# Kernel tuning notes

Hardware: AMD Instinct MI355X
Metric: run time of the kernel (lower is better)

## Reference

```python
import jax, jax.numpy as jnp
import numpy as np

D = 128; H = 4; DK = D // H; ZN = 64; V = 8

def _silu(x):
    return x * jax.nn.sigmoid(x)

def _mlp3(x, w1, b1, w2, b2, w3, b3):
    h = _silu(x @ w1 + b1)
    h = _silu(h @ w2 + b2)
    return h @ w3 + b3

def _snorm(x):
    # StaticLayerNorm: center, divide by unbiased std (torch .std default ddof=1)
    c = x - jnp.mean(x, axis=-1, keepdims=True)
    std = jnp.sqrt(jnp.sum(c * c, axis=-1, keepdims=True) / (x.shape[-1] - 1))
    std = jnp.where(std == 0, 1.0, std)
    return c / std

def setup_inputs():
    key = jax.random.key(0)
    ks = list(jax.random.split(key, 40)); ki = iter(ks)
    xs = (6.0 / (DK + D)) ** 0.5
    inp = {}
    inp["latent"] = jax.random.normal(next(ki), (ZN, D, V, V, V), jnp.float32)
    inp["nodes"] = jax.random.normal(next(ki), (ZN, D), jnp.float32)
    inp["t"] = jax.random.uniform(next(ki), (ZN,), jnp.float32)
    for nm in ("qw", "kw", "vw"):
        inp[nm] = jax.random.uniform(next(ki), (H, D, DK), jnp.float32, -xs, xs)
    for nm in ("qb", "kb", "vb"):
        inp[nm] = jnp.zeros((H, DK), jnp.float32)
    inp["ow"] = jax.random.normal(next(ki), (D, D), jnp.float32) * (1.0 / D) ** 0.5
    for pre, dout in (("an_gb", 2 * D), ("an_a", D), ("fn_gb", 2 * D), ("fn_a", D)):
        inp[pre + "_w1"] = jax.random.normal(next(ki), (D, D), jnp.float32) * 0.05
        inp[pre + "_b1"] = jnp.zeros((D,), jnp.float32)
        inp[pre + "_w2"] = jax.random.normal(next(ki), (D, D), jnp.float32) * 0.05
        inp[pre + "_b2"] = jnp.zeros((D,), jnp.float32)
        inp[pre + "_w3"] = jax.random.normal(next(ki), (D, dout), jnp.float32) * 0.05
        inp[pre + "_b3"] = jnp.zeros((dout,), jnp.float32)
    return inp

def reference(latent, nodes, t, qw, kw, vw, qb, kb, vb, ow,
              an_gb_w1, an_gb_b1, an_gb_w2, an_gb_b2, an_gb_w3, an_gb_b3,
              an_a_w1, an_a_b1, an_a_w2, an_a_b2, an_a_w3, an_a_b3,
              fn_gb_w1, fn_gb_b1, fn_gb_w2, fn_gb_b2, fn_gb_w3, fn_gb_b3,
              fn_a_w1, fn_a_b1, fn_a_w2, fn_a_b2, fn_a_w3, fn_a_b3):
    b, d, vx, vy, vz = latent.shape
    n = vx * vy * vz
    x = latent.reshape(b, d, n).transpose(0, 2, 1)  # [b, n, d]
    cond = nodes[:, None, :] + t[:, None, None]     # [b, 1, d]
    gb1 = _mlp3(cond, an_gb_w1, an_gb_b1, an_gb_w2, an_gb_b2, an_gb_w3, an_gb_b3)
    g1, be1 = jnp.split(gb1, 2, axis=-1)
    al1 = _mlp3(cond, an_a_w1, an_a_b1, an_a_w2, an_a_b2, an_a_w3, an_a_b3)
    gb2 = _mlp3(cond, fn_gb_w1, fn_gb_b1, fn_gb_w2, fn_gb_b2, fn_gb_w3, fn_gb_b3)
    g2, be2 = jnp.split(gb2, 2, axis=-1)
    al2 = _mlp3(cond, fn_a_w1, fn_a_b1, fn_a_w2, fn_a_b2, fn_a_w3, fn_a_b3)
    # FAITHFUL BUG REPRO: source unpacks adaLN's (gamma, beta, alpha) as (alpha, gamma, beta)
    alpha1, gamma1, beta1 = g1, be1, al1
    alpha2, gamma2, beta2 = g2, be2, al2
    x2 = gamma1 * _snorm(x) + beta1
    dk = d // qw.shape[0]
    Q = jnp.einsum('bnd,hdk->bhnk', x2, qw) + qb[None, :, None, :]
    K = jnp.einsum('bnd,hdk->bhnk', x2, kw) + kb[None, :, None, :]
    Vv = jnp.einsum('bnd,hdk->bhnk', x2, vw) + vb[None, :, None, :]
    S = jnp.einsum('bhnk,bhmk->bhnm', Q, K) / (dk ** 0.5)
    P = jax.nn.softmax(S, axis=-1)
    O = jnp.einsum('bhnm,bhmk->bhnk', P, Vv)
    O = O.transpose(0, 2, 3, 1).reshape(b, n, d)  # matches torch permute(0,2,3,1).reshape
    attn = O @ ow
    x = x + alpha1 * attn
    x2 = gamma2 * _snorm(x) + beta2
    x = x + alpha2 * x2  # NOTE: source forward never applies self.ffn (dead module)
    return x.transpose(0, 2, 1).reshape(b, d, vx, vy, vz)
```

## Files before the change

### kernel.cpp

```cpp
#include <hip/hip_runtime.h>
#include <hip/hip_bf16.h>
#include <math.h>


#define NB 64

typedef __attribute__((ext_vector_type(8))) short bf16x8;
typedef __attribute__((ext_vector_type(4))) float f32x4;

__device__ __forceinline__ float silu_f(float x) { return x / (1.0f + __expf(-x)); }
__device__ __forceinline__ unsigned short f2bf(float x) {
    __hip_bfloat16 h = __float2bfloat16(x);
    return *reinterpret_cast<unsigned short*>(&h);
}

__global__ void __launch_bounds__(128) k_cond(
    const float* __restrict__ nodes, const float* __restrict__ tv,
    const float* __restrict__ w10, const float* __restrict__ b10,
    const float* __restrict__ w20, const float* __restrict__ b20,
    const float* __restrict__ w30, const float* __restrict__ b30,
    const float* __restrict__ w11, const float* __restrict__ b11,
    const float* __restrict__ w21, const float* __restrict__ b21,
    const float* __restrict__ w31, const float* __restrict__ b31,
    const float* __restrict__ w12, const float* __restrict__ b12,
    const float* __restrict__ w22, const float* __restrict__ b22,
    const float* __restrict__ w32, const float* __restrict__ b32,
    const float* __restrict__ w13, const float* __restrict__ b13,
    const float* __restrict__ w23, const float* __restrict__ b23,
    const float* __restrict__ w33, const float* __restrict__ b33,
    float* __restrict__ mods,
    const float* __restrict__ qw, const float* __restrict__ kw,
    const float* __restrict__ vw, const float* __restrict__ ow,
    unsigned short* __restrict__ cT, unsigned short* __restrict__ owT)
{
    int blk = blockIdx.x;
    int t = threadIdx.x;

    if (blk >= NB*4) {
        int pbase = (blk - NB*4)*128 + t;
        #pragma unroll
        for (int rep = 0; rep < 2; rep++) {
            int idx = pbase + rep*32768;
            if (idx < 49152) {
                int ph = idx >> 14, r = idx & 16383, c = r >> 7, d = r & 127;
                int h = c >> 5, kk = c & 31;
                const float* wp = ph==0 ? qw : (ph==1 ? kw : vw);
                cT[idx] = f2bf(wp[h*4096 + d*32 + kk]);
            } else {
                int r = idx - 49152, c = r >> 7, i = r & 127;
                owT[r] = f2bf(ow[i*128 + c]);
            }
        }
        return;
    }

    int b = blk >> 2, m = blk & 3;
    const float* W1 = m==0?w10 : m==1?w11 : m==2?w12 : w13;
    const float* B1 = m==0?b10 : m==1?b11 : m==2?b12 : b13;
    const float* W2 = m==0?w20 : m==1?w21 : m==2?w22 : w23;
    const float* B2 = m==0?b20 : m==1?b21 : m==2?b22 : b23;
    const float* W3 = m==0?w30 : m==1?w31 : m==2?w32 : w33;
    const float* B3 = m==0?b30 : m==1?b31 : m==2?b32 : b33;
    int dout256 = (m == 0 || m == 2);
    int slot = (m==0)?0 : (m==1)?2 : (m==2)?3 : 5;

    __shared__ float xs[128], h1[128], h2[128];
    xs[t] = nodes[b*128 + t] + tv[b];
    __syncthreads();

    float acc = B1[t];
    for (int i = 0; i < 128; i++) acc += xs[i] * W1[i*128 + t];
    h1[t] = silu_f(acc);
    __syncthreads();

    acc = B2[t];
    for (int i = 0; i < 128; i++) acc += h1[i] * W2[i*128 + t];
    h2[t] = silu_f(acc);
    __syncthreads();

    if (dout256) {
        float a0 = B3[t], a1 = B3[t + 128];
        for (int i = 0; i < 128; i++) {
            float h = h2[i];
            a0 += h * W3[i*256 + t];
            a1 += h * W3[i*256 + t + 128];
        }
        mods[((size_t)b*6 + slot    )*128 + t] = a0;
        mods[((size_t)b*6 + slot + 1)*128 + t] = a1;
    } else {
        float a0 = B3[t];
        for (int i = 0; i < 128; i++) a0 += h2[i] * W3[i*128 + t];
        mods[((size_t)b*6 + slot)*128 + t] = a0;
    }
}

__global__ void __launch_bounds__(256, 3) k_norm_qkv(
    const float* __restrict__ latent, const float* __restrict__ mods,
    const unsigned short* __restrict__ cT,
    const float* __restrict__ qb, const float* __restrict__ kb, const float* __restrict__ vb,
    unsigned short* __restrict__ Qb, unsigned short* __restrict__ Kb,
    unsigned short* __restrict__ Vtb)
{
    __shared__ unsigned short xb[64*136];
    __shared__ unsigned short WtS[128*136];

    int blk = blockIdx.x;
    int b = blk >> 3, n0 = (blk & 7) * 64;
    int t = threadIdx.x;
    int j = t >> 2, sub = t & 3;

    const float* lp = latent + (size_t)b*65536 + n0 + j;
    float lat[32];
    #pragma unroll
    for (int i = 0; i < 32; i++)
        lat[i] = lp[(size_t)(sub*32 + i)*512];

    float s = 0.f, ss = 0.f;
    #pragma unroll
    for (int i = 0; i < 32; i++) { s += lat[i]; ss += lat[i]*lat[i]; }
    s += __shfl_xor(s, 1); ss += __shfl_xor(ss, 1);
    s += __shfl_xor(s, 2); ss += __shfl_xor(ss, 2);
    float mean = s * (1.0f/128.0f);
    float var = (ss - 128.0f*mean*mean) * (1.0f/127.0f);
    var = var < 0.f ? 0.f : var;
    float sd = sqrtf(var);
    float rstd = (sd == 0.f) ? 1.f : 1.f/sd;

    const float* g1p  = mods + ((size_t)b*6 + 1)*128 + sub*32;
    const float* be1p = mods + ((size_t)b*6 + 2)*128 + sub*32;
    unsigned int* xbw = (unsigned int*)xb + j*68 + sub*16;
    #pragma unroll
    for (int i2 = 0; i2 < 16; i2++) {
        float v0 = g1p[2*i2]   * ((lat[2*i2]   - mean)*rstd) + be1p[2*i2];
        float v1 = g1p[2*i2+1] * ((lat[2*i2+1] - mean)*rstd) + be1p[2*i2+1];
        xbw[i2] = (unsigned)f2bf(v0) | ((unsigned)f2bf(v1) << 16);
    }
    __syncthreads();

    int w = t >> 6, lane = t & 63, lo = lane & 15, hi = lane >> 4;
    bf16x8 af[4];
    #pragma unroll
    for (int kc = 0; kc < 4; kc++)
        af[kc] = *(const bf16x8*)(xb + (w*16 + lo)*136 + kc*32 + hi*8);

    const f32x4 zero = {0.f, 0.f, 0.f, 0.f};
    const float qscale = 0.17677669529663687f * 1.4426950408889634f;
    unsigned int* WtSw = (unsigned int*)WtS;

    #pragma unroll 1
    for (int ph = 0; ph < 3; ph++) {
        __syncthreads();
        {
            const uint4* cq = (const uint4*)(cT + ph*16384);
            #pragma unroll
            for (int k = 0; k < 8; k++) {
                int idx4 = t + k*256;
                int c = idx4 >> 4, d2b = (idx4 & 15)*4;
                uint4 v = cq[idx4];
                *(uint4*)(WtSw + c*68 + d2b) = v;
            }
        }
        __syncthreads();

        for (int nt = 0; nt < 8; nt++) {
            f32x4 acc = zero;
            #pragma unroll
            for (int kc = 0; kc < 4; kc++) {
                bf16x8 bf = *(const bf16x8*)(WtS + (nt*16 + lo)*136 + kc*32 + hi*8);
                acc = __builtin_amdgcn_mfma_f32_16x16x32_bf16(af[kc], bf, acc, 0, 0, 0);
            }
            int c = nt*16 + lo, h = c >> 5, kk = c & 31;
            size_t bh = (size_t)(b*4 + h);
            if (ph == 0) {
                float bias = qb[c];
                #pragma unroll
                for (int jj = 0; jj < 4; jj++) {
                    int n = n0 + w*16 + hi*4 + jj;
                    Qb[(bh*512 + n)*32 + kk] = f2bf((acc[jj] + bias) * qscale);
                }
            } else if (ph == 1) {
                float bias = kb[c];
                #pragma unroll
                for (int jj = 0; jj < 4; jj++) {
                    int n = n0 + w*16 + hi*4 + jj;
                    Kb[(bh*512 + n)*32 + kk] = f2bf(acc[jj] + bias);
                }
            } else {
                float bias = vb[c];
                #pragma unroll
                for (int jj = 0; jj < 4; jj++) {
                    int nl = w*16 + hi*4 + jj;
                    xb[c*68 + nl] = f2bf(acc[jj] + bias);
                }
            }
        }
    }
    __syncthreads();
    for (int idx = t; idx < 8192; idx += 256) {
        int c = idx >> 6, jj = idx & 63;
        int h = c >> 5, kk = c & 31;
        size_t bh = (size_t)(b*4 + h);
        Vtb[(bh*32 + kk)*512 + n0 + jj] = xb[c*68 + jj];
    }
}

__global__ void __launch_bounds__(512, 4) k_attn(
    const unsigned short* __restrict__ Qb, const unsigned short* __restrict__ Kb,
    const unsigned short* __restrict__ Vtb, unsigned short* __restrict__ Ob)
{
    __shared__ unsigned short KsS[512*32];
    __shared__ unsigned short VsS[32*512];

    int blk = blockIdx.x;
    int bh = blk >> 1, qhalf = blk & 1;
    int t = threadIdx.x;

    const unsigned short* kgp = Kb + (size_t)bh*512*32;
    const unsigned short* vgp = Vtb + (size_t)bh*32*512;
    for (int idx = t; idx < 2048; idx += 512)
        *(bf16x8*)(KsS + idx*8) = *(const bf16x8*)(kgp + idx*8);
    for (int idx = t; idx < 2048; idx += 512) {
        int r = idx >> 6, cch = idx & 63;
        *(bf16x8*)(VsS + r*512 + ((cch*8) ^ ((r&7)<<3))) =
            *(const bf16x8*)(vgp + r*512 + cch*8);
    }
    __syncthreads();

    int w = t >> 6, lane = t & 63, lo = lane & 15, hi = lane >> 4;
    const unsigned short* qbase = Qb + (size_t)bh*512*32;
    const f32x4 zero = {0.f, 0.f, 0.f, 0.f};
    int b = bh >> 2, h = bh & 3;

    const unsigned short* Vl0 = VsS + lo*512;
    const unsigned short* Vl1 = VsS + (16 + lo)*512;
    int swz = (lo & 7) << 3;
    int srcA = lo + 32*(hi & 1);

    for (int qt = 0; qt < 2; ++qt) {
        int q0 = qhalf*256 + w*32 + qt*16;
        bf16x8 qa = *(const bf16x8*)(qbase + (size_t)(q0 + lo)*32 + hi*8);

        float m = -1e30f, sum = 0.f;
        f32x4 oa = zero, ob = zero;

        #pragma unroll 1
        for (int ch = 0; ch < 4; ++ch) {
            f32x4 s8[8];
            #pragma unroll
            for (int kt = 0; kt < 8; ++kt) {
                bf16x8 kf = *(const bf16x8*)(KsS + ((ch*8 + kt)*16 + lo)*32 + hi*8);
                s8[kt] = __builtin_amdgcn_mfma_f32_16x16x32_bf16(kf, qa, zero, 0, 0, 0);
            }

            float cm = -1e30f;
            #pragma unroll
            for (int kt = 0; kt < 8; ++kt)
                cm = fmaxf(cm, fmaxf(fmaxf(s8[kt][0], s8[kt][1]), fmaxf(s8[kt][2], s8[kt][3])));
            cm = fmaxf(cm, __shfl_xor(cm, 16));
            cm = fmaxf(cm, __shfl_xor(cm, 32));
            float nm = fmaxf(m, cm);
            float sc = __builtin_amdgcn_exp2f(m - nm);
            sum *= sc;
            #pragma unroll
            for (int jj = 0; jj < 4; ++jj) { oa[jj] *= sc; ob[jj] *= sc; }
            m = nm;

            unsigned pw0c[8], pw1c[8];
            #pragma unroll
            for (int kt = 0; kt < 8; ++kt) {
                float p0 = __builtin_amdgcn_exp2f(s8[kt][0] - nm);
                float p1 = __builtin_amdgcn_exp2f(s8[kt][1] - nm);
                float p2 = __builtin_amdgcn_exp2f(s8[kt][2] - nm);
                float p3 = __builtin_amdgcn_exp2f(s8[kt][3] - nm);
                sum += (p0 + p1) + (p2 + p3);
                pw0c[kt] = (unsigned)f2bf(p0) | ((unsigned)f2bf(p1) << 16);
                pw1c[kt] = (unsigned)f2bf(p2) | ((unsigned)f2bf(p3) << 16);
            }

            #pragma unroll
            for (int kt2 = 0; kt2 < 4; ++kt2) {
                unsigned e0 = pw0c[2*kt2],     e1 = pw1c[2*kt2];
                unsigned o0 = pw0c[2*kt2 + 1], o1 = pw1c[2*kt2 + 1];
                unsigned ae0 = (unsigned)__shfl((int)e0, srcA, 64);
                unsigned ae1 = (unsigned)__shfl((int)e1, srcA, 64);
                unsigned ao0 = (unsigned)__shfl((int)o0, srcA, 64);
                unsigned ao1 = (unsigned)__shfl((int)o1, srcA, 64);
                unsigned be0 = (unsigned)__shfl((int)e0, srcA + 16, 64);
                unsigned be1 = (unsigned)__shfl((int)e1, srcA + 16, 64);
                unsigned bo0 = (unsigned)__shfl((int)o0, srcA + 16, 64);
                unsigned bo1 = (unsigned)__shfl((int)o1, srcA + 16, 64);
                union { unsigned u[4]; bf16x8 v; } pb;
                pb.u[0] = (hi < 2) ? ae0 : ao0;
                pb.u[1] = (hi < 2) ? ae1 : ao1;
                pb.u[2] = (hi < 2) ? be0 : bo0;
                pb.u[3] = (hi < 2) ? be1 : bo1;
                int off = (((ch*4 + kt2)*32) + hi*8) ^ swz;
                bf16x8 v0 = *(const bf16x8*)(Vl0 + off);
                bf16x8 v1 = *(const bf16x8*)(Vl1 + off);
                oa = __builtin_amdgcn_mfma_f32_16x16x32_bf16(v0, pb.v, oa, 0, 0, 0);
                ob = __builtin_amdgcn_mfma_f32_16x16x32_bf16(v1, pb.v, ob, 0, 0, 0);
            }
        }

        sum += __shfl_xor(sum, 16);
        sum += __shfl_xor(sum, 32);

        float inv = 1.f / sum;
        unsigned short* op = Ob + ((size_t)(b*512 + q0 + lo))*128 + h;
        #pragma unroll
        for (int jj = 0; jj < 4; ++jj) {
            op[(hi*4 + jj)*4]       = f2bf(oa[jj] * inv);
            op[(16 + hi*4 + jj)*4]  = f2bf(ob[jj] * inv);
        }
    }
}

__global__ void __launch_bounds__(256, 2) k_out(
    const float* __restrict__ latent, const unsigned short* __restrict__ Ob,
    const unsigned short* __restrict__ owT, const float* __restrict__ mods,
    float* __restrict__ outp)
{
    __shared__ unsigned short owS[128*136];
    __shared__ float xs[64*129];
    __shared__ float a1s[128], a2s[128], g2s[128], b2s[128];
    __shared__ float mean_s[64], rstd_s[64];

    int blk = blockIdx.x;
    int b = blk >> 3, n0 = (blk & 7) * 64;
    int t = threadIdx.x;

    if (t < 128) {
        a1s[t] = mods[((size_t)b*6 + 0)*128 + t];
        a2s[t] = mods[((size_t)b*6 + 3)*128 + t];
        g2s[t] = mods[((size_t)b*6 + 4)*128 + t];
        b2s[t] = mods[((size_t)b*6 + 5)*128 + t];
    }
    {
        unsigned int* owSw = (unsigned int*)owS;
        const uint4* oq = (const uint4*)owT;
        #pragma unroll
        for (int k = 0; k < 8; k++) {
            int idx4 = t + k*256;
            int c = idx4 >> 4, d2b = (idx4 & 15)*4;
            uint4 v = oq[idx4];
            *(uint4*)(owSw + c*68 + d2b) = v;
        }
    }
    const float* lp = latent + (size_t)b*65536 + n0;
    for (int idx = t; idx < 8192; idx += 256) {
        int d = idx >> 6, jj = idx & 63;
        xs[jj*129 + d] = lp[(size_t)d*512 + jj];
    }
    __syncthreads();

    int w = t >> 6, lane = t & 63, lo = lane & 15, hi = lane >> 4;

    const unsigned short* arow = Ob + ((size_t)(b*512 + n0 + w*16 + lo))*128;
    bf16x8 af[4];
    #pragma unroll
    for (int kc = 0; kc < 4; kc++)
        af[kc] = *(const bf16x8*)(arow + kc*32 + hi*8);

    const f32x4 zero = {0.f, 0.f, 0.f, 0.f};
    for (int nt = 0; nt < 8; nt++) {
        f32x4 acc = zero;
        #pragma unroll
        for (int kc = 0; kc < 4; kc++) {
            bf16x8 bf = *(const bf16x8*)(owS + (nt*16 + lo)*136 + kc*32 + hi*8);
            acc = __builtin_amdgcn_mfma_f32_16x16x32_bf16(af[kc], bf, acc, 0, 0, 0);
        }
        int c = nt*16 + lo;
        #pragma unroll
        for (int jj = 0; jj < 4; jj++) {
            int nl = w*16 + hi*4 + jj;
            xs[nl*129 + c] += a1s[c] * acc[jj];
        }
    }
    __syncthreads();

    {
        int row = t >> 2, sub = t & 3;
        float s = 0.f, ss = 0.f;
        const float* xr = &xs[row*129 + sub*32];
        #pragma unroll
        for (int i = 0; i < 32; i++) { float v = xr[i]; s += v; ss += v*v; }
        s += __shfl_xor(s, 1); ss += __shfl_xor(ss, 1);
        s += __shfl_xor(s, 2); ss += __shfl_xor(ss, 2);
        float mean = s * (1.0f/128.0f);
        float var = (ss - 128.0f*mean*mean) * (1.0f/127.0f);
        var = var < 0.f ? 0.f : var;
        float sd = sqrtf(var);
        mean_s[row] = mean;
        rstd_s[row] = (sd == 0.f) ? 1.f : 1.f/sd;
    }
    __syncthreads();

    float* outb = outp + (size_t)b*65536 + n0;
    for (int idx = t; idx < 8192; idx += 256) {
        int d = idx >> 6, jj = idx & 63;
        float v = xs[jj*129 + d];
        float nv = (v - mean_s[jj]) * rstd_s[jj];
        outb[(size_t)d*512 + jj] = v + a2s[d]*(g2s[d]*nv + b2s[d]);
    }
}

extern "C" void kernel_launch(void* const* d_in, const int* in_sizes, int n_in,
                              void* d_out, int out_size, void* d_ws, size_t ws_size,
                              hipStream_t stream) {
    const float* latent = (const float*)d_in[0];
    const float* nodes  = (const float*)d_in[1];
    const float* tv     = (const float*)d_in[2];
    const float* qw     = (const float*)d_in[3];
    const float* kw     = (const float*)d_in[4];
    const float* vw     = (const float*)d_in[5];
    const float* qb     = (const float*)d_in[6];
    const float* kb     = (const float*)d_in[7];
    const float* vb     = (const float*)d_in[8];
    const float* owp    = (const float*)d_in[9];

    const float* mw[24];
    for (int i = 0; i < 24; i++) mw[i] = (const float*)d_in[10 + i];

    char* wsb = (char*)d_ws;
    unsigned short* Qb  = (unsigned short*)(wsb);
    unsigned short* Kb  = (unsigned short*)(wsb + 8388608);
    unsigned short* Vtb = (unsigned short*)(wsb + 16777216);
    unsigned short* Ob  = (unsigned short*)(wsb + 25165824);
    float* mods         = (float*)(wsb + 33554432);
    unsigned short* cT  = (unsigned short*)(wsb + 33751040);
    unsigned short* owT = (unsigned short*)(wsb + 33849344);

    float* outp = (float*)d_out;

    k_cond<<<dim3(NB*4 + 256), dim3(128), 0, stream>>>(
        nodes, tv,
        mw[0], mw[1], mw[2], mw[3], mw[4], mw[5],
        mw[6], mw[7], mw[8], mw[9], mw[10], mw[11],
        mw[12], mw[13], mw[14], mw[15], mw[16], mw[17],
        mw[18], mw[19], mw[20], mw[21], mw[22], mw[23],
        mods,
        qw, kw, vw, owp, cT, owT);

    k_norm_qkv<<<dim3(NB*8), dim3(256), 0, stream>>>(
        latent, mods, cT, qb, kb, vb, Qb, Kb, Vtb);

    k_attn<<<dim3(NB*4*2), dim3(512), 0, stream>>>(Qb, Kb, Vtb, Ob);

    k_out<<<dim3(NB*8), dim3(256), 0, stream>>>(latent, Ob, owT, mods, outp);
}
```

Before: 200.8 us.

## Vectorize out-kernel I/O, pack attention stores, add lazy softmax rescale

The out kernel now loads latent and stores output with float4 accesses instead of scalar strided ones. The attention kernel writes each head's output as packed contiguous uint2 words, so O is laid out head-contiguous. The ow transpose is permuted to match that layout. Softmax now skips the running-max rescale when the chunk max grows by at most 8 (log2 domain), which saves exp and multiply work but lets probabilities reach up to 2^8 before the bf16 conversion.

```diff
diff --git a/kernel.cpp b/kernel.cpp
--- a/kernel.cpp
+++ b/kernel.cpp
@@ -47,7 +47,8 @@
                 const float* wp = ph==0 ? qw : (ph==1 ? kw : vw);
                 cT[idx] = f2bf(wp[h*4096 + d*32 + kk]);
             } else {
-                int r = idx - 49152, c = r >> 7, i = r & 127;
+                int r = idx - 49152, c = r >> 7, sc = r & 127;
+                int i = (sc & 31)*4 + (sc >> 5);
                 owT[r] = f2bf(ow[i*128 + c]);
             }
         }
@@ -258,20 +259,22 @@
                 cm = fmaxf(cm, fmaxf(fmaxf(s8[kt][0], s8[kt][1]), fmaxf(s8[kt][2], s8[kt][3])));
             cm = fmaxf(cm, __shfl_xor(cm, 16));
             cm = fmaxf(cm, __shfl_xor(cm, 32));
-            float nm = fmaxf(m, cm);
-            float sc = __builtin_amdgcn_exp2f(m - nm);
-            sum *= sc;
-            #pragma unroll
-            for (int jj = 0; jj < 4; ++jj) { oa[jj] *= sc; ob[jj] *= sc; }
-            m = nm;
+            if (!__all(cm - m <= 8.0f)) {
+                float nm = fmaxf(m, cm);
+                float sc = __builtin_amdgcn_exp2f(m - nm);
+                sum *= sc;
+                #pragma unroll
+                for (int jj = 0; jj < 4; ++jj) { oa[jj] *= sc; ob[jj] *= sc; }
+                m = nm;
+            }
 
             unsigned pw0c[8], pw1c[8];
             #pragma unroll
             for (int kt = 0; kt < 8; ++kt) {
-                float p0 = __builtin_amdgcn_exp2f(s8[kt][0] - nm);
-                float p1 = __builtin_amdgcn_exp2f(s8[kt][1] - nm);
-                float p2 = __builtin_amdgcn_exp2f(s8[kt][2] - nm);
-                float p3 = __builtin_amdgcn_exp2f(s8[kt][3] - nm);
+                float p0 = __builtin_amdgcn_exp2f(s8[kt][0] - m);
+                float p1 = __builtin_amdgcn_exp2f(s8[kt][1] - m);
+                float p2 = __builtin_amdgcn_exp2f(s8[kt][2] - m);
+                float p3 = __builtin_amdgcn_exp2f(s8[kt][3] - m);
                 sum += (p0 + p1) + (p2 + p3);
                 pw0c[kt] = (unsigned)f2bf(p0) | ((unsigned)f2bf(p1) << 16);
                 pw1c[kt] = (unsigned)f2bf(p2) | ((unsigned)f2bf(p3) << 16);
@@ -306,12 +309,14 @@
         sum += __shfl_xor(sum, 32);
 
         float inv = 1.f / sum;
-        unsigned short* op = Ob + ((size_t)(b*512 + q0 + lo))*128 + h;
-        #pragma unroll
-        for (int jj = 0; jj < 4; ++jj) {
-            op[(hi*4 + jj)*4]       = f2bf(oa[jj] * inv);
-            op[(16 + hi*4 + jj)*4]  = f2bf(ob[jj] * inv);
-        }
+        unsigned int* opw = (unsigned int*)(Ob + ((size_t)(b*512 + q0 + lo))*128 + h*32);
+        uint2 ua, ub;
+        ua.x = (unsigned)f2bf(oa[0]*inv) | ((unsigned)f2bf(oa[1]*inv) << 16);
+        ua.y = (unsigned)f2bf(oa[2]*inv) | ((unsigned)f2bf(oa[3]*inv) << 16);
+        ub.x = (unsigned)f2bf(ob[0]*inv) | ((unsigned)f2bf(ob[1]*inv) << 16);
+        ub.y = (unsigned)f2bf(ob[2]*inv) | ((unsigned)f2bf(ob[3]*inv) << 16);
+        *(uint2*)(opw + hi*2)     = ua;
+        *(uint2*)(opw + 8 + hi*2) = ub;
     }
 }
 
@@ -347,9 +352,13 @@
         }
     }
     const float* lp = latent + (size_t)b*65536 + n0;
-    for (int idx = t; idx < 8192; idx += 256) {
-        int d = idx >> 6, jj = idx & 63;
-        xs[jj*129 + d] = lp[(size_t)d*512 + jj];
+    for (int idx = t; idx < 2048; idx += 256) {
+        int d = idx >> 4, j4 = (idx & 15)*4;
+        float4 v = *(const float4*)(lp + (size_t)d*512 + j4);
+        xs[(j4+0)*129 + d] = v.x;
+        xs[(j4+1)*129 + d] = v.y;
+        xs[(j4+2)*129 + d] = v.z;
+        xs[(j4+3)*129 + d] = v.w;
     }
     __syncthreads();
 
@@ -396,11 +405,26 @@
     __syncthreads();
 
     float* outb = outp + (size_t)b*65536 + n0;
-    for (int idx = t; idx < 8192; idx += 256) {
-        int d = idx >> 6, jj = idx & 63;
-        float v = xs[jj*129 + d];
-        float nv = (v - mean_s[jj]) * rstd_s[jj];
-        outb[(size_t)d*512 + jj] = v + a2s[d]*(g2s[d]*nv + b2s[d]);
+    for (int idx = t; idx < 2048; idx += 256) {
+        int d = idx >> 4, j4 = (idx & 15)*4;
+        float4 o;
+        {
+            float v = xs[(j4+0)*129 + d];
+            o.x = v + a2s[d]*(g2s[d]*((v - mean_s[j4+0])*rstd_s[j4+0]) + b2s[d]);
+        }
+        {
+            float v = xs[(j4+1)*129 + d];
+            o.y = v + a2s[d]*(g2s[d]*((v - mean_s[j4+1])*rstd_s[j4+1]) + b2s[d]);
+        }
+        {
+            float v = xs[(j4+2)*129 + d];
+            o.z = v + a2s[d]*(g2s[d]*((v - mean_s[j4+2])*rstd_s[j4+2]) + b2s[d]);
+        }
+        {
+            float v = xs[(j4+3)*129 + d];
+            o.w = v + a2s[d]*(g2s[d]*((v - mean_s[j4+3])*rstd_s[j4+3]) + b2s[d]);
+        }
+        *(float4*)(outb + (size_t)d*512 + j4) = o;
     }
 }
 
```

Result: no change. 198.9 us (-1.0%).
